# Kernel tuning notes

Measured on AMD Instinct MI355X. Metric: run time of the kernel, lower is better.

Reference implementation:

```python
import jax, jax.numpy as jnp
import numpy as np

N_NODES = 100000

def setup_inputs() -> dict:
    key = jax.random.key(0)
    ks = jax.random.split(key, 8)
    n_feat, nhid, nclass = 256, 128, 40
    n_edges = 1600000
    x = jax.random.normal(ks[0], (N_NODES, n_feat), dtype=jnp.float32)
    edge_index = jax.random.randint(ks[1], (2, n_edges), 0, N_NODES, dtype=jnp.int64)
    # Glorot-ish scaled weights
    W1 = jax.random.normal(ks[2], (n_feat, nhid), dtype=jnp.float32) / np.sqrt(n_feat)
    b1 = jnp.zeros((nhid,), dtype=jnp.float32)
    W2 = jax.random.normal(ks[3], (nhid, nhid), dtype=jnp.float32) / np.sqrt(nhid)
    b2 = jnp.zeros((nhid,), dtype=jnp.float32)
    Wc = jax.random.normal(ks[4], (nhid, nclass), dtype=jnp.float32) / np.sqrt(nhid)
    bc = jnp.zeros((nclass,), dtype=jnp.float32)
    return {"x": x, "edge_index": edge_index, "W1": W1, "b1": b1,
            "W2": W2, "b2": b2, "Wc": Wc, "bc": bc}


def _gcn_conv(x, src, dst, W, b, n_nodes):
    """PyG GCNConv: transform, then sym-normalized aggregation with self-loops.
    out_i = sum_{j in N(i) u {i}} (d_i^-1/2 d_j^-1/2) (x_j W) + b,
    where d = in-degree over A + I.
    """
    h = x @ W  # [N, out]
    ones = jnp.ones_like(dst, dtype=h.dtype)
    deg = jax.ops.segment_sum(ones, dst, num_segments=n_nodes) + 1.0  # + self loop
    dinv = jax.lax.rsqrt(deg)  # deg >= 1, always valid
    norm = dinv[src] * dinv[dst]  # [E]
    msg = h[src] * norm[:, None]  # [E, out]  (dominant gather traffic)
    agg = jax.ops.segment_sum(msg, dst, num_segments=n_nodes)
    agg = agg + h * (dinv * dinv)[:, None]  # self-loop contribution
    return agg + b


def reference(x, edge_index, W1, b1, W2, b2, Wc, bc):
    # eval mode: dropout is identity
    src, dst = edge_index[0], edge_index[1]
    n = x.shape[0]
    h = jax.nn.relu(_gcn_conv(x, src, dst, W1, b1, n))
    h = jax.nn.relu(_gcn_conv(h, src, dst, W2, b2, n))
    return h @ Wc + bc
```

## Files before the change

### kernel.cpp

```cpp
#include <hip/hip_runtime.h>
#include <hip/hip_bf16.h>
#include <hip/hip_fp16.h>
#include <type_traits>


typedef _Float16 half8 __attribute__((ext_vector_type(8)));
typedef _Float16 half4v __attribute__((ext_vector_type(4)));
typedef float floatx4 __attribute__((ext_vector_type(4)));

#define EPB 8192


__device__ inline int block_incl_scan_256(int t, int* tmp) {
    int tid = threadIdx.x;
    tmp[tid] = t;
    __syncthreads();
    #pragma unroll
    for (int off = 1; off < 256; off <<= 1) {
        int v = (tid >= off) ? tmp[tid - off] : 0;
        __syncthreads();
        tmp[tid] += v;
        __syncthreads();
    }
    return tmp[tid];
}

template <int ITEMS>
__global__ __launch_bounds__(256) void k_scan1(const int* __restrict__ v,
                                               int* __restrict__ bsum, int n) {
    __shared__ int tmp[256];
    int base = blockIdx.x * (256 * ITEMS) + threadIdx.x * ITEMS;
    int t = 0;
    #pragma unroll
    for (int l = 0; l < ITEMS; ++l) {
        int i = base + l;
        t += (i < n) ? v[i] : 0;
    }
    block_incl_scan_256(t, tmp);
    if (threadIdx.x == 0) bsum[blockIdx.x] = tmp[255];
}

__global__ __launch_bounds__(256) void k_scan2(int* __restrict__ bsum, int nb) {
    __shared__ int tmp[256];
    int tid = threadIdx.x;
    int v = (tid < nb) ? bsum[tid] : 0;
    block_incl_scan_256(v, tmp);
    if (tid < nb) bsum[tid] = tid ? tmp[tid - 1] : 0;
}

template <int ITEMS>
__global__ __launch_bounds__(256) void k_scan3(const int* __restrict__ vin,
                                               const int* __restrict__ bsum,
                                               int* __restrict__ rp, int n) {
    __shared__ int tmp[256];
    int base = blockIdx.x * (256 * ITEMS) + threadIdx.x * ITEMS;
    int v[ITEMS];
    int t = 0;
    #pragma unroll
    for (int l = 0; l < ITEMS; ++l) {
        int i = base + l;
        v[l] = (i < n) ? vin[i] : 0;
        t += v[l];
    }
    block_incl_scan_256(t, tmp);
    int run = bsum[blockIdx.x] + (threadIdx.x ? tmp[threadIdx.x - 1] : 0);
    #pragma unroll
    for (int l = 0; l < ITEMS; ++l) {
        int i = base + l;
        if (i < n) rp[i] = run;
        run += v[l];
    }
}


__global__ __launch_bounds__(256) void k_histA(const int* __restrict__ dst,
                                               int* __restrict__ histM,
                                               int E, int nblk) {
    __shared__ int h[512];
    int tid = threadIdx.x;
    for (int i = tid; i < 512; i += 256) h[i] = 0;
    __syncthreads();
    int base = blockIdx.x * EPB;
    #pragma unroll 4
    for (int l = 0; l < EPB / 256; ++l) {
        int i = base + l * 256 + tid;
        if (i < E) atomicAdd(&h[dst[i] >> 8], 1);
    }
    __syncthreads();
    for (int i = tid; i < 512; i += 256)
        histM[i * nblk + blockIdx.x] = h[i];
}

__global__ __launch_bounds__(256) void k_scatterA(const int* __restrict__ src,
                                                  const int* __restrict__ dst,
                                                  const int* __restrict__ histS,
                                                  unsigned long long* __restrict__ eB,
                                                  int E, int nblk) {
    __shared__ int bse[512];
    __shared__ int cnt[512];
    int tid = threadIdx.x;
    for (int i = tid; i < 512; i += 256) {
        bse[i] = histS[i * nblk + blockIdx.x];
        cnt[i] = 0;
    }
    __syncthreads();
    int base = blockIdx.x * EPB;
    #pragma unroll 4
    for (int l = 0; l < EPB / 256; ++l) {
        int i = base + l * 256 + tid;
        if (i < E) {
            int d = dst[i];
            int s = src[i];
            int b = d >> 8;
            int r = atomicAdd(&cnt[b], 1);
            eB[bse[b] + r] = ((unsigned long long)(unsigned)d << 32) | (unsigned)s;
        }
    }
}

#define BCAP 4608
__global__ __launch_bounds__(256) void k_sortB(const unsigned long long* __restrict__ eB,
                                               const int* __restrict__ histS,
                                               int* __restrict__ srcS,
                                               int* __restrict__ rowptr,
                                               float* __restrict__ dinv,
                                               int n, int E, int nblk) {
    const int b   = blockIdx.x;
    const int tid = threadIdx.x;
    const int ni0 = b << 8;
    int s0 = histS[b * nblk];
    int s1 = (b < 511) ? histS[(b + 1) * nblk] : E;
    int cnt = s1 - s0;
    if (cnt > BCAP) cnt = BCAP;
    if (cnt == 0 && ni0 > n) return;

    __shared__ int hist[256];
    __shared__ int tmp[256];
    __shared__ int baseA[256];
    __shared__ int cntA[256];
    __shared__ int dstL[BCAP];
    __shared__ unsigned srcL[BCAP];
    __shared__ int lbA[256];

    hist[tid] = 0;
    cntA[tid] = 0;
    __syncthreads();
    for (int i = s0 + tid; i < s0 + cnt; i += 256) {
        int d = (int)(eB[i] >> 32);
        atomicAdd(&hist[d & 255], 1);
    }
    __syncthreads();
    int own  = hist[tid];
    int incl = block_incl_scan_256(own, tmp);
    baseA[tid] = incl - own;
    __syncthreads();
    for (int i = s0 + tid; i < s0 + cnt; i += 256) {
        unsigned long long v = eB[i];
        int d = (int)(v >> 32);
        int dig = d & 255;
        int r = atomicAdd(&cntA[dig], 1);
        int pos = baseA[dig] + r;
        dstL[pos] = d;
        srcL[pos] = (unsigned)v;
    }
    __syncthreads();
    for (int j = tid; j < cnt; j += 256)
        srcS[s0 + j] = (int)srcL[j];
    if (ni0 <= n) {
        int i = ni0 + tid;
        int lo = 0, hi = cnt;
        while (lo < hi) {
            int mid = (lo + hi) >> 1;
            if (dstL[mid] < i) lo = mid + 1; else hi = mid;
        }
        lbA[tid] = lo;
        __syncthreads();
        if (i <= n) {
            rowptr[i] = s0 + lo;
            if (i < n) {
                int ub = (tid < 255) ? lbA[tid + 1] : cnt;
                dinv[i] = rsqrtf((float)(ub - lo + 1));
            }
        }
    }
}

__global__ __launch_bounds__(256) void k_wcast(const float* __restrict__ W,
                                               _Float16* __restrict__ Wt,
                                               int N, int K, int kbits, int total) {
    int i = blockIdx.x * 256 + threadIdx.x;
    if (i < total) {
        int c = i >> kbits;
        int k = i & (K - 1);
        Wt[i] = (c < N) ? (_Float16)W[(size_t)k * N + c] : (_Float16)0.f;
    }
}


template <int K, int BN, int MT, typename AT, typename OT>
__global__ __launch_bounds__(256) void gemm_bres(const AT* __restrict__ A,
                                                 const _Float16* __restrict__ Wt,
                                                 const float* __restrict__ bias,
                                                 OT* __restrict__ C,
                                                 int M, int N) {
    constexpr int KP = K + 8;
    constexpr int NT = BN / 16;
    __shared__ __align__(16) _Float16 Bs[BN * KP];

    const int tid  = threadIdx.x;
    const int lane = tid & 63;
    const int wv   = tid >> 6;
    const int qd   = lane >> 4;
    const int ln15 = lane & 15;
    const int bm   = blockIdx.x * (64 * MT);

    constexpr int TOT = BN * K / 8;
    for (int i = tid; i < TOT; i += 256) {
        int idx = i * 8;
        int col = idx / K;
        int kk  = idx % K;
        *(uint4*)&Bs[col * KP + kk] = *(const uint4*)(Wt + idx);
    }
    __syncthreads();

    floatx4 acc[MT][NT];
    #pragma unroll
    for (int mt = 0; mt < MT; ++mt)
        #pragma unroll
        for (int c = 0; c < NT; ++c) acc[mt][c] = (floatx4){0.f, 0.f, 0.f, 0.f};

    int rw[MT];
    #pragma unroll
    for (int mt = 0; mt < MT; ++mt) {
        int r = bm + (wv * MT + mt) * 16 + ln15;
        rw[mt] = (r < M) ? r : (M - 1);
    }

    #pragma unroll
    for (int ks = 0; ks < K / 32; ++ks) {
        half8 a[MT];
        #pragma unroll
        for (int mt = 0; mt < MT; ++mt) {
            if constexpr (std::is_same<AT, float>::value) {
                const float* p = A + (size_t)rw[mt] * K + ks * 32 + qd * 8;
                float4 v0 = *(const float4*)p;
                float4 v1 = *(const float4*)(p + 4);
                half8 h;
                h[0] = (_Float16)v0.x; h[1] = (_Float16)v0.y;
                h[2] = (_Float16)v0.z; h[3] = (_Float16)v0.w;
                h[4] = (_Float16)v1.x; h[5] = (_Float16)v1.y;
                h[6] = (_Float16)v1.z; h[7] = (_Float16)v1.w;
                a[mt] = h;
            } else {
                a[mt] = *(const half8*)((const _Float16*)A +
                                        (size_t)rw[mt] * K + ks * 32 + qd * 8);
            }
        }
        #pragma unroll
        for (int c = 0; c < NT; ++c) {
            half8 b = *(const half8*)&Bs[(c * 16 + ln15) * KP + ks * 32 + qd * 8];
            #pragma unroll
            for (int mt = 0; mt < MT; ++mt)
                acc[mt][c] = __builtin_amdgcn_mfma_f32_16x16x32_f16(a[mt], b,
                                                                    acc[mt][c], 0, 0, 0);
        }
    }

    #pragma unroll
    for (int mt = 0; mt < MT; ++mt) {
        int baseRow = bm + (wv * MT + mt) * 16 + qd * 4;
        #pragma unroll
        for (int c = 0; c < NT; ++c) {
            int col = c * 16 + ln15;
            if constexpr (std::is_same<OT, _Float16>::value) {
                #pragma unroll
                for (int r = 0; r < 4; ++r) {
                    int row = baseRow + r;
                    if (row < M) C[(size_t)row * N + col] = (_Float16)acc[mt][c][r];
                }
            } else {
                float bv = (col < N && bias) ? bias[col] : 0.f;
                #pragma unroll
                for (int r = 0; r < 4; ++r) {
                    int row = baseRow + r;
                    if (row < M && col < N)
                        ((float*)C)[(size_t)row * N + col] = acc[mt][c][r] + bv;
                }
            }
        }
    }
}


__global__ __launch_bounds__(256) void gcn_agg(const unsigned int* __restrict__ h,
                                               const int* __restrict__ rowptr,
                                               const int* __restrict__ srcS,
                                               const float* __restrict__ dinv,
                                               const float* __restrict__ bias,
                                               unsigned int* __restrict__ out,
                                               int n, int do_relu) {
    int node = blockIdx.x * 4 + (threadIdx.x >> 6);
    if (node >= n) return;
    const int lane = threadIdx.x & 63;
    const int g    = lane >> 4;
    const int t    = lane & 15;

    const _Float16* hb = (const _Float16*)h;

    float di = dinv[node];
    int e0 = rowptr[node];
    int e1 = rowptr[node + 1];

    half8 sv = *(const half8*)(hb + (size_t)(unsigned)node * 128 + t * 8);
    const float4* b4 = (const float4*)bias;
    float4 blo = b4[t * 2 + 0];
    float4 bhi = b4[t * 2 + 1];

    float acc[8];
    #pragma unroll
    for (int i = 0; i < 8; ++i) acc[i] = 0.f;

    for (int ce = e0; ce < e1; ce += 64) {
        int cnt = e1 - ce;
        cnt = (cnt < 64) ? cnt : 64;
        int colv = 0, wval = 0;
        if (lane < cnt) {
            int c = srcS[ce + lane];
            colv = c;
            wval = __float_as_int(di * dinv[c]);
        }
        int d = 0;
        for (; d + 16 <= cnt; d += 16) {
            int i0 = (d + 0 + g) << 2;
            int i1 = (d + 4 + g) << 2;
            int i2 = (d + 8 + g) << 2;
            int i3 = (d + 12 + g) << 2;
            int c0 = __builtin_amdgcn_ds_bpermute(i0, colv);
            int c1 = __builtin_amdgcn_ds_bpermute(i1, colv);
            int c2 = __builtin_amdgcn_ds_bpermute(i2, colv);
            int c3 = __builtin_amdgcn_ds_bpermute(i3, colv);
            int w0i = __builtin_amdgcn_ds_bpermute(i0, wval);
            int w1i = __builtin_amdgcn_ds_bpermute(i1, wval);
            int w2i = __builtin_amdgcn_ds_bpermute(i2, wval);
            int w3i = __builtin_amdgcn_ds_bpermute(i3, wval);
            half8 h0 = *(const half8*)(hb + (size_t)(unsigned)c0 * 128 + t * 8);
            half8 h1 = *(const half8*)(hb + (size_t)(unsigned)c1 * 128 + t * 8);
            half8 h2 = *(const half8*)(hb + (size_t)(unsigned)c2 * 128 + t * 8);
            half8 h3 = *(const half8*)(hb + (size_t)(unsigned)c3 * 128 + t * 8);
            float w0 = __int_as_float(w0i);
            float w1 = __int_as_float(w1i);
            float w2 = __int_as_float(w2i);
            float w3 = __int_as_float(w3i);
            #pragma unroll
            for (int i = 0; i < 8; ++i) acc[i] += (float)h0[i] * w0;
            #pragma unroll
            for (int i = 0; i < 8; ++i) acc[i] += (float)h1[i] * w1;
            #pragma unroll
            for (int i = 0; i < 8; ++i) acc[i] += (float)h2[i] * w2;
            #pragma unroll
            for (int i = 0; i < 8; ++i) acc[i] += (float)h3[i] * w3;
        }
        for (; d < cnt; d += 4) {
            int idx = (d + g) << 2;
            int c   = __builtin_amdgcn_ds_bpermute(idx, colv);
            float w = __int_as_float(__builtin_amdgcn_ds_bpermute(idx, wval));
            half8 hv = *(const half8*)(hb + (size_t)(unsigned)c * 128 + t * 8);
            #pragma unroll
            for (int i = 0; i < 8; ++i)
                acc[i] += (float)hv[i] * w;
        }
    }

    #pragma unroll
    for (int i = 0; i < 8; ++i) acc[i] += __shfl_xor(acc[i], 16);
    #pragma unroll
    for (int i = 0; i < 8; ++i) acc[i] += __shfl_xor(acc[i], 32);

    float s = di * di;
    float bb[8] = {blo.x, blo.y, blo.z, blo.w, bhi.x, bhi.y, bhi.z, bhi.w};
    half8 o;
    #pragma unroll
    for (int i = 0; i < 8; ++i) {
        float v = acc[i] + (float)sv[i] * s + bb[i];
        if (do_relu) v = fmaxf(v, 0.f);
        o[i] = (_Float16)v;
    }
    if (g == 0)
        *(half8*)((_Float16*)out + (size_t)(unsigned)node * 128 + t * 8) = o;
}


extern "C" void kernel_launch(void* const* d_in, const int* in_sizes, int n_in,
                              void* d_out, int out_size, void* d_ws, size_t ws_size,
                              hipStream_t stream) {
    const float* x  = (const float*)d_in[0];
    const int* eidx = (const int*)d_in[1];
    const float* W1 = (const float*)d_in[2];
    const float* b1 = (const float*)d_in[3];
    const float* W2 = (const float*)d_in[4];
    const float* b2 = (const float*)d_in[5];
    const float* Wc = (const float*)d_in[6];
    const float* bc = (const float*)d_in[7];
    float* out = (float*)d_out;

    const int NF = 256, NH = 128, NC = 40;
    const int n = in_sizes[0] / NF;
    const int E = in_sizes[1] / 2;
    const int* src = eidx;
    const int* dst = eidx + E;

    const int nblk = (E + EPB - 1) / EPB;
    const int hm   = 512 * nblk;
    const int nbA  = (hm + 4095) / 4096;

    char* wsb = (char*)d_ws;
    size_t off = 0;
    auto alloc = [&](size_t bytes) {
        char* p = wsb + off;
        off = (off + bytes + 511) & ~(size_t)511;
        return p;
    };
    _Float16* hbuf = (_Float16*)alloc((size_t)n * NH * 2);
    _Float16* abuf = (_Float16*)alloc((size_t)n * NH * 2);
    _Float16* W1t  = (_Float16*)alloc((size_t)128 * 256 * 2);
    _Float16* W2t  = (_Float16*)alloc((size_t)128 * 128 * 2);
    _Float16* Wct  = (_Float16*)alloc((size_t)48 * 128 * 2);
    unsigned long long* eB = (unsigned long long*)alloc((size_t)E * 8);
    int* srcS      = (int*)alloc((size_t)E * 4);
    int* histM     = (int*)alloc((size_t)hm * 4);
    int* histS     = (int*)alloc((size_t)hm * 4);
    int* rowptr    = (int*)alloc((size_t)(n + 1) * 4);
    float* dinv    = (float*)alloc((size_t)n * 4);
    int* bsumA     = (int*)alloc(1024);

    k_histA<<<nblk, 256, 0, stream>>>(dst, histM, E, nblk);
    k_scan1<16><<<nbA, 256, 0, stream>>>(histM, bsumA, hm);
    k_scan2<<<1, 256, 0, stream>>>(bsumA, nbA);
    k_scan3<16><<<nbA, 256, 0, stream>>>(histM, bsumA, histS, hm);
    k_scatterA<<<nblk, 256, 0, stream>>>(src, dst, histS, eB, E, nblk);
    k_sortB<<<512, 256, 0, stream>>>(eB, histS, srcS, rowptr, dinv, n, E, nblk);

    k_wcast<<<(128 * 256 + 255) / 256, 256, 0, stream>>>(W1, W1t, 128, 256, 8, 128 * 256);
    k_wcast<<<(128 * 128 + 255) / 256, 256, 0, stream>>>(W2, W2t, 128, 128, 7, 128 * 128);
    k_wcast<<<(48 * 128 + 255) / 256, 256, 0, stream>>>(Wc, Wct, 40, 128, 7, 48 * 128);

    const int gB = (n + 127) / 128;
    gemm_bres<256, 128, 2, float, _Float16><<<gB, 256, 0, stream>>>(x, W1t, nullptr, hbuf, n, NH);
    gcn_agg<<<(n + 3) / 4, 256, 0, stream>>>((const unsigned int*)hbuf, rowptr, srcS, dinv, b1,
                                             (unsigned int*)abuf, n, 1);
    gemm_bres<128, 128, 2, _Float16, _Float16><<<gB, 256, 0, stream>>>(abuf, W2t, nullptr, hbuf, n, NH);
    gcn_agg<<<(n + 3) / 4, 256, 0, stream>>>((const unsigned int*)hbuf, rowptr, srcS, dinv, b2,
                                             (unsigned int*)abuf, n, 1);
    gemm_bres<128, 48, 2, _Float16, float><<<gB, 256, 0, stream>>>(abuf, Wct, bc, out, n, NC);
}
```

Measured before the change: 421.0 us.

## Merge weight casts, chunk GEMM K into LDS halves, simplify aggregation loop

Fuses the three weight-transpose/cast kernels into one launch. The GEMM now stages the weight tile in LDS in K-chunks of at most 128, which halves shared memory for the K=256 layer and should allow more resident blocks, at the cost of an extra barrier and reload per chunk. The aggregation kernel drops its 4-edge manual unroll for a simpler unroll-2 loop with packed half2-to-float2 conversion. That cuts register pressure but may expose fewer concurrent gathers per wave.

```diff
diff --git a/kernel.cpp b/kernel.cpp
--- a/kernel.cpp
+++ b/kernel.cpp
@@ -185,14 +185,24 @@
     }
 }
 
-__global__ __launch_bounds__(256) void k_wcast(const float* __restrict__ W,
-                                               _Float16* __restrict__ Wt,
-                                               int N, int K, int kbits, int total) {
+__global__ __launch_bounds__(256) void k_wcast_all(const float* __restrict__ W1,
+                                                   _Float16* __restrict__ W1t,
+                                                   const float* __restrict__ W2,
+                                                   _Float16* __restrict__ W2t,
+                                                   const float* __restrict__ Wc,
+                                                   _Float16* __restrict__ Wct) {
     int i = blockIdx.x * 256 + threadIdx.x;
-    if (i < total) {
-        int c = i >> kbits;
-        int k = i & (K - 1);
-        Wt[i] = (c < N) ? (_Float16)W[(size_t)k * N + c] : (_Float16)0.f;
+    if (i < 32768) {
+        int c = i >> 8, k = i & 255;
+        W1t[i] = (_Float16)W1[(size_t)k * 128 + c];
+    } else if (i < 32768 + 16384) {
+        int j = i - 32768;
+        int c = j >> 7, k = j & 127;
+        W2t[j] = (_Float16)W2[(size_t)k * 128 + c];
+    } else if (i < 32768 + 16384 + 6144) {
+        int j = i - 32768 - 16384;
+        int c = j >> 7, k = j & 127;
+        Wct[j] = (c < 40) ? (_Float16)Wc[(size_t)k * 40 + c] : (_Float16)0.f;
     }
 }
 
@@ -203,7 +213,8 @@
                                                  const float* __restrict__ bias,
                                                  OT* __restrict__ C,
                                                  int M, int N) {
-    constexpr int KP = K + 8;
+    constexpr int KC = (K > 128) ? 128 : K;
+    constexpr int KP = KC + 8;
     constexpr int NT = BN / 16;
     __shared__ __align__(16) _Float16 Bs[BN * KP];
 
@@ -214,15 +225,6 @@
     const int ln15 = lane & 15;
     const int bm   = blockIdx.x * (64 * MT);
 
-    constexpr int TOT = BN * K / 8;
-    for (int i = tid; i < TOT; i += 256) {
-        int idx = i * 8;
-        int col = idx / K;
-        int kk  = idx % K;
-        *(uint4*)&Bs[col * KP + kk] = *(const uint4*)(Wt + idx);
-    }
-    __syncthreads();
-
     floatx4 acc[MT][NT];
     #pragma unroll
     for (int mt = 0; mt < MT; ++mt)
@@ -237,33 +239,48 @@
     }
 
     #pragma unroll
-    for (int ks = 0; ks < K / 32; ++ks) {
-        half8 a[MT];
+    for (int kh = 0; kh < K; kh += KC) {
+        constexpr int TOT = BN * KC / 8;
+        for (int i = tid; i < TOT; i += 256) {
+            int idx = i * 8;
+            int col = idx / KC;
+            int kk  = idx % KC;
+            *(uint4*)&Bs[col * KP + kk] =
+                *(const uint4*)(Wt + (size_t)col * K + kh + kk);
+        }
+        __syncthreads();
+
         #pragma unroll
-        for (int mt = 0; mt < MT; ++mt) {
-            if constexpr (std::is_same<AT, float>::value) {
-                const float* p = A + (size_t)rw[mt] * K + ks * 32 + qd * 8;
-                float4 v0 = *(const float4*)p;
-                float4 v1 = *(const float4*)(p + 4);
-                half8 h;
-                h[0] = (_Float16)v0.x; h[1] = (_Float16)v0.y;
-                h[2] = (_Float16)v0.z; h[3] = (_Float16)v0.w;
-                h[4] = (_Float16)v1.x; h[5] = (_Float16)v1.y;
-                h[6] = (_Float16)v1.z; h[7] = (_Float16)v1.w;
-                a[mt] = h;
-            } else {
-                a[mt] = *(const half8*)((const _Float16*)A +
-                                        (size_t)rw[mt] * K + ks * 32 + qd * 8);
+        for (int ks = 0; ks < KC / 32; ++ks) {
+            const int k0 = kh + ks * 32;
+            half8 a[MT];
+            #pragma unroll
+            for (int mt = 0; mt < MT; ++mt) {
+                if constexpr (std::is_same<AT, float>::value) {
+                    const float* p = A + (size_t)rw[mt] * K + k0 + qd * 8;
+                    float4 v0 = *(const float4*)p;
+                    float4 v1 = *(const float4*)(p + 4);
+                    half8 h;
+                    h[0] = (_Float16)v0.x; h[1] = (_Float16)v0.y;
+                    h[2] = (_Float16)v0.z; h[3] = (_Float16)v0.w;
+                    h[4] = (_Float16)v1.x; h[5] = (_Float16)v1.y;
+                    h[6] = (_Float16)v1.z; h[7] = (_Float16)v1.w;
+                    a[mt] = h;
+                } else {
+                    a[mt] = *(const half8*)((const _Float16*)A +
+                                            (size_t)rw[mt] * K + k0 + qd * 8);
+                }
             }
-        }
-        #pragma unroll
-        for (int c = 0; c < NT; ++c) {
-            half8 b = *(const half8*)&Bs[(c * 16 + ln15) * KP + ks * 32 + qd * 8];
             #pragma unroll
-            for (int mt = 0; mt < MT; ++mt)
-                acc[mt][c] = __builtin_amdgcn_mfma_f32_16x16x32_f16(a[mt], b,
-                                                                    acc[mt][c], 0, 0, 0);
-        }
+            for (int c = 0; c < NT; ++c) {
+                half8 b = *(const half8*)&Bs[(c * 16 + ln15) * KP + ks * 32 + qd * 8];
+                #pragma unroll
+                for (int mt = 0; mt < MT; ++mt)
+                    acc[mt][c] = __builtin_amdgcn_mfma_f32_16x16x32_f16(a[mt], b,
+                                                                        acc[mt][c], 0, 0, 0);
+            }
+        }
+        __syncthreads();
     }
 
     #pragma unroll
@@ -292,6 +309,11 @@
 }
 
 
+static __device__ __forceinline__ float2 h2f2u(unsigned int raw) {
+    __half2 h = *(__half2*)&raw;
+    return __half22float2(h);
+}
+
 __global__ __launch_bounds__(256) void gcn_agg(const unsigned int* __restrict__ h,
                                                const int* __restrict__ rowptr,
                                                const int* __restrict__ srcS,
@@ -316,9 +338,9 @@
     float4 blo = b4[t * 2 + 0];
     float4 bhi = b4[t * 2 + 1];
 
-    float acc[8];
-    #pragma unroll
-    for (int i = 0; i < 8; ++i) acc[i] = 0.f;
+    float2 acc[4];
+    #pragma unroll
+    for (int i = 0; i < 4; ++i) acc[i] = make_float2(0.f, 0.f);
 
     for (int ce = e0; ce < e1; ce += 64) {
         int cnt = e1 - ce;
@@ -329,59 +351,38 @@
             colv = c;
             wval = __float_as_int(di * dinv[c]);
         }
-        int d = 0;
-        for (; d + 16 <= cnt; d += 16) {
-            int i0 = (d + 0 + g) << 2;
-            int i1 = (d + 4 + g) << 2;
-            int i2 = (d + 8 + g) << 2;
-            int i3 = (d + 12 + g) << 2;
-            int c0 = __builtin_amdgcn_ds_bpermute(i0, colv);
-            int c1 = __builtin_amdgcn_ds_bpermute(i1, colv);
-            int c2 = __builtin_amdgcn_ds_bpermute(i2, colv);
-            int c3 = __builtin_amdgcn_ds_bpermute(i3, colv);
-            int w0i = __builtin_amdgcn_ds_bpermute(i0, wval);
-            int w1i = __builtin_amdgcn_ds_bpermute(i1, wval);
-            int w2i = __builtin_amdgcn_ds_bpermute(i2, wval);
-            int w3i = __builtin_amdgcn_ds_bpermute(i3, wval);
-            half8 h0 = *(const half8*)(hb + (size_t)(unsigned)c0 * 128 + t * 8);
-            half8 h1 = *(const half8*)(hb + (size_t)(unsigned)c1 * 128 + t * 8);
-            half8 h2 = *(const half8*)(hb + (size_t)(unsigned)c2 * 128 + t * 8);
-            half8 h3 = *(const half8*)(hb + (size_t)(unsigned)c3 * 128 + t * 8);
-            float w0 = __int_as_float(w0i);
-            float w1 = __int_as_float(w1i);
-            float w2 = __int_as_float(w2i);
-            float w3 = __int_as_float(w3i);
-            #pragma unroll
-            for (int i = 0; i < 8; ++i) acc[i] += (float)h0[i] * w0;
-            #pragma unroll
-            for (int i = 0; i < 8; ++i) acc[i] += (float)h1[i] * w1;
-            #pragma unroll
-            for (int i = 0; i < 8; ++i) acc[i] += (float)h2[i] * w2;
-            #pragma unroll
-            for (int i = 0; i < 8; ++i) acc[i] += (float)h3[i] * w3;
-        }
-        for (; d < cnt; d += 4) {
+        #pragma unroll 2
+        for (int d = 0; d < cnt; d += 4) {
             int idx = (d + g) << 2;
             int c   = __builtin_amdgcn_ds_bpermute(idx, colv);
             float w = __int_as_float(__builtin_amdgcn_ds_bpermute(idx, wval));
-            half8 hv = *(const half8*)(hb + (size_t)(unsigned)c * 128 + t * 8);
-            #pragma unroll
-            for (int i = 0; i < 8; ++i)
-                acc[i] += (float)hv[i] * w;
-        }
-    }
-
-    #pragma unroll
-    for (int i = 0; i < 8; ++i) acc[i] += __shfl_xor(acc[i], 16);
-    #pragma unroll
-    for (int i = 0; i < 8; ++i) acc[i] += __shfl_xor(acc[i], 32);
+            const unsigned* hp = (const unsigned*)(hb + (size_t)(unsigned)c * 128 + t * 8);
+            uint4 hv = *(const uint4*)hp;
+            float2 u0 = h2f2u(hv.x);
+            float2 u1 = h2f2u(hv.y);
+            float2 u2 = h2f2u(hv.z);
+            float2 u3 = h2f2u(hv.w);
+            acc[0].x += u0.x * w; acc[0].y += u0.y * w;
+            acc[1].x += u1.x * w; acc[1].y += u1.y * w;
+            acc[2].x += u2.x * w; acc[2].y += u2.y * w;
+            acc[3].x += u3.x * w; acc[3].y += u3.y * w;
+        }
+    }
+
+    #pragma unroll
+    for (int i = 0; i < 4; ++i) {
+        acc[i].x += __shfl_xor(acc[i].x, 16);
+        acc[i].y += __shfl_xor(acc[i].y, 16);
+        acc[i].x += __shfl_xor(acc[i].x, 32);
+        acc[i].y += __shfl_xor(acc[i].y, 32);
+    }
 
     float s = di * di;
     float bb[8] = {blo.x, blo.y, blo.z, blo.w, bhi.x, bhi.y, bhi.z, bhi.w};
     half8 o;
     #pragma unroll
     for (int i = 0; i < 8; ++i) {
-        float v = acc[i] + (float)sv[i] * s + bb[i];
+        float v = ((i & 1) ? acc[i >> 1].y : acc[i >> 1].x) + (float)sv[i] * s + bb[i];
         if (do_relu) v = fmaxf(v, 0.f);
         o[i] = (_Float16)v;
     }
@@ -440,9 +441,8 @@
     k_scatterA<<<nblk, 256, 0, stream>>>(src, dst, histS, eB, E, nblk);
     k_sortB<<<512, 256, 0, stream>>>(eB, histS, srcS, rowptr, dinv, n, E, nblk);
 
-    k_wcast<<<(128 * 256 + 255) / 256, 256, 0, stream>>>(W1, W1t, 128, 256, 8, 128 * 256);
-    k_wcast<<<(128 * 128 + 255) / 256, 256, 0, stream>>>(W2, W2t, 128, 128, 7, 128 * 128);
-    k_wcast<<<(48 * 128 + 255) / 256, 256, 0, stream>>>(Wc, Wct, 40, 128, 7, 48 * 128);
+    k_wcast_all<<<(32768 + 16384 + 6144 + 255) / 256, 256, 0, stream>>>(
+        W1, W1t, W2, W2t, Wc, Wct);
 
     const int gB = (n + 127) / 128;
     gemm_bres<256, 128, 2, float, _Float16><<<gB, 256, 0, stream>>>(x, W1t, nullptr, hbuf, n, NH);
```

After: 413.8 us. Within noise of the previous version (-1.7%).
